# Performance work log

Hardware: AMD Instinct MI355X
Metric: run time of the kernel (lower is better)

The kernel has to match this reference:

```python
import jax, jax.numpy as jnp
import numpy as np

H, DK, DV, DEMB = 16, 64, 64, 1024
D_MODEL = H * DV


def setup_inputs() -> dict:
    key = jax.random.key(0)
    ks = jax.random.split(key, 9)
    scale = 0.02
    x = jax.random.normal(ks[0], (4, 2048, DEMB), dtype=jnp.float32)
    wq = jax.random.normal(ks[1], (DEMB, H * DK), dtype=jnp.float32) * scale
    bq = jnp.zeros((H * DK,), dtype=jnp.float32)
    wk = jax.random.normal(ks[2], (DEMB, H * DK), dtype=jnp.float32) * scale
    bk = jnp.zeros((H * DK,), dtype=jnp.float32)
    wv = jax.random.normal(ks[3], (DEMB, H * DV), dtype=jnp.float32) * scale
    bv = jnp.zeros((H * DV,), dtype=jnp.float32)
    wo = jax.random.normal(ks[4], (D_MODEL, D_MODEL), dtype=jnp.float32) * scale
    bo = jnp.zeros((D_MODEL,), dtype=jnp.float32)
    return {"x": x, "wq": wq, "bq": bq, "wk": wk, "bk": bk,
            "wv": wv, "bv": bv, "wo": wo, "bo": bo, "mask": 0}


def _split_heads(t, h):
    # (b, s, h*d) -> (b, h, s, d)
    b, s, _ = t.shape
    return t.reshape(b, s, h, -1).transpose(0, 2, 1, 3)


def reference(x, wq, bq, wk, bk, wv, bv, wo, bo, mask):
    b, s, _ = x.shape
    qs = _split_heads(x @ wq + bq, H)  # (b, h, s, dk)
    ks = _split_heads(x @ wk + bk, H)
    vs = _split_heads(x @ wv + bv, H)  # (b, h, s, dv)
    # FAITHFUL quirk: original scales by 1/sqrt(len(ks[0])) == 1/sqrt(n_heads),
    # not 1/sqrt(d_k).
    scores = jnp.einsum('bhqd,bhkd->bhqk', qs, ks) / jnp.sqrt(jnp.float32(H))
    # FAITHFUL quirk: masked_fill(mask == 0, ...) with scalar bool mask is a
    # no-op (True == 0 is False), so no masking is ever applied.
    attn = jax.nn.softmax(scores, axis=-1)
    out = jnp.einsum('bhqk,bhkd->bhqd', attn, vs)  # (b, h, s, dv)
    out = out.transpose(0, 2, 1, 3).reshape(b, s, D_MODEL)
    return out @ wo + bo
```

## Files before the change

kernel.cpp:

```cpp
#include <hip/hip_runtime.h>
#include <stdint.h>

typedef __attribute__((ext_vector_type(8))) short short8;
typedef __attribute__((ext_vector_type(4))) short short4v;
typedef __attribute__((ext_vector_type(4))) float floatx4;
typedef __attribute__((ext_vector_type(4))) _Float16 half4;
typedef __attribute__((ext_vector_type(2))) __fp16 pk2;

#define SEQ 2048
#define NTOK 8192
#define QSCALE 0.360673760222241f

#define MFMA16F16(a,b,c) __builtin_amdgcn_mfma_f32_16x16x16f16((a),(b),(c),0,0,0)

__device__ __forceinline__ float b2f(unsigned short u){
  union { unsigned int i; float f; } v; v.i = ((unsigned int)u) << 16; return v.f;
}
__device__ __forceinline__ unsigned short f2b(float f){
  union { float f; unsigned int i; } v; v.f = f;
  unsigned int r = v.i + 0x7fffu + ((v.i >> 16) & 1u);
  return (unsigned short)(r >> 16);
}
__device__ __forceinline__ void async16(const unsigned short* g, unsigned short* l){
  __builtin_amdgcn_global_load_lds(
      (const __attribute__((address_space(1))) unsigned int*)g,
      (__attribute__((address_space(3))) unsigned int*)l, 16, 0, 0);
}

__global__ __launch_bounds__(256) void convert_x_kernel(
    const float* __restrict__ src, unsigned short* __restrict__ dst)
{
  int i = (blockIdx.x*256 + threadIdx.x)*4;
  float4 v = *(const float4*)(src + i);
  short4v o;
  o[0] = (short)f2b(v.x); o[1] = (short)f2b(v.y);
  o[2] = (short)f2b(v.z); o[3] = (short)f2b(v.w);
  *(short4v*)(dst + i) = o;
}

__global__ __launch_bounds__(256) void transpose_w_kernel(
    const float* __restrict__ wq, const float* __restrict__ wk,
    const float* __restrict__ wv, const float* __restrict__ wo,
    unsigned short* __restrict__ wqkvT, unsigned short* __restrict__ woT)
{
  __shared__ unsigned short lT[64][72];
  const int sel = blockIdx.z;
  const float* src = (sel==0)?wq:(sel==1)?wk:(sel==2)?wv:wo;
  unsigned short* dst = (sel<3) ? (wqkvT + (size_t)sel*1024*1024) : woT;
  const int n0 = blockIdx.x * 64, k0 = blockIdx.y * 64;
  const int tid = threadIdx.x;
#pragma unroll
  for (int i=0;i<4;i++){
    int ch = tid + i*256;
    int r = ch>>4, c = (ch&15)*4;
    float4 v = *(const float4*)(src + (size_t)(k0+r)*1024 + n0 + c);
    lT[r][c+0] = f2b(v.x); lT[r][c+1] = f2b(v.y);
    lT[r][c+2] = f2b(v.z); lT[r][c+3] = f2b(v.w);
  }
  __syncthreads();
#pragma unroll
  for (int i=0;i<2;i++){
    int ch = tid + i*256;
    int rn = ch>>3, c = (ch&7)*8;
    short8 v;
#pragma unroll
    for (int j=0;j<8;j++) v[j] = (short)lT[c+j][rn];
    *(short8*)(dst + (size_t)(n0+rn)*1024 + k0 + c) = v;
  }
}

__global__ void bias_concat_kernel(const float* __restrict__ bq,
                                   const float* __restrict__ bk,
                                   const float* __restrict__ bv,
                                   float* __restrict__ bqkv){
  int i = blockIdx.x*256 + threadIdx.x;
  if (i < 3072){
    int sel = i >> 10, j = i & 1023;
    bqkv[i] = (sel==0)?bq[j]:(sel==1)?bk[j]:bv[j];
  }
}

template<int OUT_F32, int SCALE_Q>
__global__ __launch_bounds__(256) void gemm_bt_kernel(
    const unsigned short* __restrict__ A,
    const unsigned short* __restrict__ Bt,
    const float* __restrict__ bias,
    void* __restrict__ Cv,
    int M, int N, int K)
{
  __shared__ unsigned short lA[128*64];
  __shared__ unsigned short lB[128*64];
  const int tid  = threadIdx.x;
  const int lane = tid & 63;
  const int wave = tid >> 6;
  const int quad = lane >> 4;
  const int l15  = lane & 15;
  const int wR = (wave >> 1) * 64;
  const int wC = (wave & 1) * 64;
  const int rowB = blockIdx.y * 128;
  const int colB = blockIdx.x * 128;

  const int srow = wave*32 + (lane>>3);
  const int sc8  = (lane&7) ^ (lane>>3);
  const unsigned short* gA = A  + (size_t)(rowB + srow)*K + sc8*8;
  const unsigned short* gB = Bt + (size_t)(colB + srow)*K + sc8*8;
  unsigned short* lAw = lA + wave*32*64 + lane*8;
  unsigned short* lBw = lB + wave*32*64 + lane*8;

  floatx4 acc[4][4];
#pragma unroll
  for (int t=0;t<4;t++)
#pragma unroll
    for (int u=0;u<4;u++) acc[t][u] = (floatx4){0.f,0.f,0.f,0.f};

  for (int kt = 0; kt < K; kt += 64){
    __syncthreads();
#pragma unroll
    for (int i=0;i<4;i++){
      async16(gA + (size_t)i*8*K + kt, lAw + i*512);
      async16(gB + (size_t)i*8*K + kt, lBw + i*512);
    }
    __syncthreads();
#pragma unroll
    for (int ks=0; ks<2; ks++){
      const int cph = ((ks*4 + quad) ^ (l15 & 7)) * 8;
      short8 af[4], bf[4];
#pragma unroll
      for (int t=0;t<4;t++) af[t] = *(const short8*)&lA[(wR + t*16 + l15)*64 + cph];
#pragma unroll
      for (int u=0;u<4;u++) bf[u] = *(const short8*)&lB[(wC + u*16 + l15)*64 + cph];
#pragma unroll
      for (int t=0;t<4;t++)
#pragma unroll
        for (int u=0;u<4;u++)
          acc[t][u] = __builtin_amdgcn_mfma_f32_16x16x32_bf16(af[t], bf[u], acc[t][u], 0, 0, 0);
    }
  }
#pragma unroll
  for (int u=0;u<4;u++){
    int col = colB + wC + u*16 + l15;
    float bval = bias[col];
    float scale = (SCALE_Q && col < 1024) ? QSCALE : 1.0f;
#pragma unroll
    for (int t=0;t<4;t++){
      int row0 = rowB + wR + t*16 + quad*4;
#pragma unroll
      for (int r=0;r<4;r++){
        float val = (acc[t][u][r] + bval) * scale;
        if (OUT_F32) ((float*)Cv)[(size_t)(row0 + r)*N + col] = val;
        else ((unsigned short*)Cv)[(size_t)(row0 + r)*N + col] = f2b(val);
      }
    }
  }
}

__global__ __launch_bounds__(256) void transpose_v_kernel(
    const unsigned short* __restrict__ qkv,
    unsigned short* __restrict__ vt)
{
  __shared__ unsigned short lT[64][72];
  const int bh = blockIdx.x;
  const int b = bh >> 4, h = bh & 15;
  const int s0 = blockIdx.y * 64;
  const int tid = threadIdx.x;
#pragma unroll
  for (int i=0;i<2;i++){
    int ch = tid + i*256;
    int r = ch >> 3, c = (ch & 7)*8;
    short8 raw = *(const short8*)(qkv + (size_t)(b*SEQ + s0 + r)*3072 + 2048 + h*64 + c);
#pragma unroll
    for (int j=0;j<8;j++){
      union { _Float16 h; unsigned short u; } cv;
      cv.h = (_Float16)b2f((unsigned short)raw[j]);
      lT[r][c+j] = cv.u;
    }
  }
  __syncthreads();
#pragma unroll
  for (int i=0;i<2;i++){
    int ch = tid + i*256;
    int dv = ch >> 3, c = (ch & 7)*8;
    short8 v;
#pragma unroll
    for (int j=0;j<8;j++) v[j] = (short)lT[c+j][dv];
    *(short8*)(vt + (size_t)(bh*64 + dv)*2048 + s0 + c) = v;
  }
}

__global__ __launch_bounds__(256) void flash_attn_kernel(
    const unsigned short* __restrict__ qkv,
    const unsigned short* __restrict__ vt,
    unsigned short* __restrict__ attn_out)
{
  __shared__ unsigned short sK[64][72];
  __shared__ _Float16 sVt[64][72];
  const int bh = blockIdx.x;
  const int b = bh >> 4, h = bh & 15;
  const int qt = blockIdx.y;
  const int tid = threadIdx.x;
  const int wave = tid >> 6;
  const int lane = tid & 63;
  const int quad = lane >> 4, l15 = lane & 15;
  const int tok0 = b*SEQ + qt*128;

  short8 qf[2][2];
#pragma unroll
  for (int t=0;t<2;t++)
#pragma unroll
    for (int ks=0;ks<2;ks++)
      qf[t][ks] = *(const short8*)(qkv + (size_t)(tok0 + wave*32 + t*16 + l15)*3072
                                   + h*64 + ks*32 + quad*8);

  floatx4 oacc[2][4];
  float psum[2] = {0.f, 0.f};
#pragma unroll
  for (int t=0;t<2;t++)
#pragma unroll
    for (int v=0;v<4;v++) oacc[t][v] = (floatx4){0.f,0.f,0.f,0.f};

  const int ch0 = tid, ch1 = tid + 256;
  const int r0 = ch0 >> 3, c0 = (ch0 & 7)*8;
  const int r1 = ch1 >> 3, c1 = (ch1 & 7)*8;
  short8 rk[2], rv[2];
  rk[0] = *(const short8*)(qkv + (size_t)(b*SEQ + r0)*3072 + 1024 + h*64 + c0);
  rk[1] = *(const short8*)(qkv + (size_t)(b*SEQ + r1)*3072 + 1024 + h*64 + c1);
  rv[0] = *(const short8*)(vt  + (size_t)(bh*64 + r0)*2048 + c0);
  rv[1] = *(const short8*)(vt  + (size_t)(bh*64 + r1)*2048 + c1);

  for (int it = 0; it < SEQ/64; it++){
    __syncthreads();
    *(short8*)&sK[r0][c0]  = rk[0];
    *(short8*)&sK[r1][c1]  = rk[1];
    *(short8*)&sVt[r0][c0] = rv[0];
    *(short8*)&sVt[r1][c1] = rv[1];
    __syncthreads();
    if (it + 1 < SEQ/64){
      int itn = (it + 1) * 64;
      rk[0] = *(const short8*)(qkv + (size_t)(b*SEQ + itn + r0)*3072 + 1024 + h*64 + c0);
      rk[1] = *(const short8*)(qkv + (size_t)(b*SEQ + itn + r1)*3072 + 1024 + h*64 + c1);
      rv[0] = *(const short8*)(vt  + (size_t)(bh*64 + r0)*2048 + itn + c0);
      rv[1] = *(const short8*)(vt  + (size_t)(bh*64 + r1)*2048 + itn + c1);
    }

    floatx4 sacc[4][2];
#pragma unroll
    for (int u=0;u<4;u++)
#pragma unroll
      for (int t=0;t<2;t++) sacc[u][t] = (floatx4){0.f,0.f,0.f,0.f};
#pragma unroll
    for (int ks=0;ks<2;ks++){
      short8 kf[4];
#pragma unroll
      for (int u=0;u<4;u++) kf[u] = *(const short8*)&sK[u*16 + l15][ks*32 + quad*8];
#pragma unroll
      for (int u=0;u<4;u++)
#pragma unroll
        for (int t=0;t<2;t++)
          sacc[u][t] = __builtin_amdgcn_mfma_f32_16x16x32_bf16(kf[u], qf[t][ks], sacc[u][t], 0,0,0);
    }

    half4 pf[4][2];
#pragma unroll
    for (int t=0;t<2;t++){
#pragma unroll
      for (int u=0;u<4;u++){
        float p0 = __builtin_amdgcn_exp2f(sacc[u][t][0]);
        float p1 = __builtin_amdgcn_exp2f(sacc[u][t][1]);
        float p2 = __builtin_amdgcn_exp2f(sacc[u][t][2]);
        float p3 = __builtin_amdgcn_exp2f(sacc[u][t][3]);
        psum[t] += (p0+p1)+(p2+p3);
        union { pk2 p2v[2]; half4 h4; } cv;
        cv.p2v[0] = __builtin_amdgcn_cvt_pkrtz(p0,p1);
        cv.p2v[1] = __builtin_amdgcn_cvt_pkrtz(p2,p3);
        pf[u][t] = cv.h4;
      }
    }

#pragma unroll
    for (int v=0;v<4;v++){
      half4 vf[4];
#pragma unroll
      for (int u=0;u<4;u++) vf[u] = *(const half4*)&sVt[v*16 + l15][u*16 + quad*4];
#pragma unroll
      for (int t=0;t<2;t++)
#pragma unroll
        for (int u=0;u<4;u++)
          oacc[t][v] = MFMA16F16(pf[u][t], vf[u], oacc[t][v]);
    }
  }

#pragma unroll
  for (int t=0;t<2;t++){
    float s = psum[t];
    s += __shfl_xor(s, 16);
    s += __shfl_xor(s, 32);
    psum[t] = s;
  }
#pragma unroll
  for (int t=0;t<2;t++){
#pragma unroll
    for (int r=0;r<4;r++){
      float inv = 1.0f / __shfl(psum[t], quad*4 + r);
      int tok = tok0 + wave*32 + t*16 + quad*4 + r;
#pragma unroll
      for (int v=0;v<4;v++)
        attn_out[(size_t)tok*1024 + h*64 + v*16 + l15] = f2b(oacc[t][v][r] * inv);
    }
  }
}

extern "C" void kernel_launch(void* const* d_in, const int* in_sizes, int n_in,
                              void* d_out, int out_size, void* d_ws, size_t ws_size,
                              hipStream_t stream)
{
  const float* x  = (const float*)d_in[0];
  const float* wq = (const float*)d_in[1];
  const float* bq = (const float*)d_in[2];
  const float* wk = (const float*)d_in[3];
  const float* bk = (const float*)d_in[4];
  const float* wv = (const float*)d_in[5];
  const float* bv = (const float*)d_in[6];
  const float* wo = (const float*)d_in[7];
  const float* bo = (const float*)d_in[8];
  float* out = (float*)d_out;

  char* ws = (char*)d_ws;
  unsigned short* wqkvT  = (unsigned short*)(ws);
  unsigned short* woT    = (unsigned short*)(ws + 6291456);
  float*          bqkv   = (float*)(ws + 8388608);
  unsigned short* xb     = (unsigned short*)(ws + 8400896);
  unsigned short* qkvbuf = (unsigned short*)(ws + 25178112);
  unsigned short* vtbuf  = (unsigned short*)(ws + 75509760);
  unsigned short* aobuf  = (unsigned short*)(ws + 92286976);

  convert_x_kernel<<<dim3(8192), 256, 0, stream>>>(x, xb);
  transpose_w_kernel<<<dim3(16,16,4), 256, 0, stream>>>(wq, wk, wv, wo, wqkvT, woT);
  bias_concat_kernel<<<dim3(12), 256, 0, stream>>>(bq, bk, bv, bqkv);
  gemm_bt_kernel<0,1><<<dim3(24, 64), 256, 0, stream>>>(xb, wqkvT, bqkv, qkvbuf, 8192, 3072, 1024);
  transpose_v_kernel<<<dim3(64, 32), 256, 0, stream>>>(qkvbuf, vtbuf);
  flash_attn_kernel<<<dim3(64, 16), 256, 0, stream>>>(qkvbuf, vtbuf, aobuf);
  gemm_bt_kernel<1,0><<<dim3(8, 64), 256, 0, stream>>>(aobuf, woT, bo, out, 8192, 1024, 1024);
}
```

Before: 313.1 us.

## Double-buffer flash-attention K/V tiles via async LDS loads; merge prep kernels

The flash attention kernel now stages K and V^T tiles into two LDS buffers with direct global-to-LDS async loads, using an XOR-swizzled layout in place of padded rows. This cuts the register round trip and one of the two barriers per iteration, and lets the next tile's load overlap the current tile's MFMA work. Separately, the three prep kernels (x conversion, weight transpose, bias concat) are merged into one launch to save launch overhead. The changes double LDS use and depend on correct swizzle indexing and on the async loads being complete before the barrier.

```diff
diff --git a/kernel.cpp b/kernel.cpp
--- a/kernel.cpp
+++ b/kernel.cpp
@@ -27,56 +27,56 @@
       (__attribute__((address_space(3))) unsigned int*)l, 16, 0, 0);
 }
 
-__global__ __launch_bounds__(256) void convert_x_kernel(
-    const float* __restrict__ src, unsigned short* __restrict__ dst)
-{
-  int i = (blockIdx.x*256 + threadIdx.x)*4;
-  float4 v = *(const float4*)(src + i);
-  short4v o;
-  o[0] = (short)f2b(v.x); o[1] = (short)f2b(v.y);
-  o[2] = (short)f2b(v.z); o[3] = (short)f2b(v.w);
-  *(short4v*)(dst + i) = o;
-}
-
-__global__ __launch_bounds__(256) void transpose_w_kernel(
+__global__ __launch_bounds__(256) void prep_kernel(
+    const float* __restrict__ x,
     const float* __restrict__ wq, const float* __restrict__ wk,
     const float* __restrict__ wv, const float* __restrict__ wo,
-    unsigned short* __restrict__ wqkvT, unsigned short* __restrict__ woT)
+    const float* __restrict__ bq, const float* __restrict__ bk,
+    const float* __restrict__ bv,
+    unsigned short* __restrict__ xb,
+    unsigned short* __restrict__ wqkvT, unsigned short* __restrict__ woT,
+    float* __restrict__ bqkv)
 {
   __shared__ unsigned short lT[64][72];
-  const int sel = blockIdx.z;
-  const float* src = (sel==0)?wq:(sel==1)?wk:(sel==2)?wv:wo;
-  unsigned short* dst = (sel<3) ? (wqkvT + (size_t)sel*1024*1024) : woT;
-  const int n0 = blockIdx.x * 64, k0 = blockIdx.y * 64;
+  const int bid = blockIdx.x;
   const int tid = threadIdx.x;
-#pragma unroll
-  for (int i=0;i<4;i++){
-    int ch = tid + i*256;
-    int r = ch>>4, c = (ch&15)*4;
-    float4 v = *(const float4*)(src + (size_t)(k0+r)*1024 + n0 + c);
-    lT[r][c+0] = f2b(v.x); lT[r][c+1] = f2b(v.y);
-    lT[r][c+2] = f2b(v.z); lT[r][c+3] = f2b(v.w);
-  }
-  __syncthreads();
-#pragma unroll
-  for (int i=0;i<2;i++){
-    int ch = tid + i*256;
-    int rn = ch>>3, c = (ch&7)*8;
-    short8 v;
-#pragma unroll
-    for (int j=0;j<8;j++) v[j] = (short)lT[c+j][rn];
-    *(short8*)(dst + (size_t)(n0+rn)*1024 + k0 + c) = v;
-  }
-}
-
-__global__ void bias_concat_kernel(const float* __restrict__ bq,
-                                   const float* __restrict__ bk,
-                                   const float* __restrict__ bv,
-                                   float* __restrict__ bqkv){
-  int i = blockIdx.x*256 + threadIdx.x;
-  if (i < 3072){
-    int sel = i >> 10, j = i & 1023;
-    bqkv[i] = (sel==0)?bq[j]:(sel==1)?bk[j]:bv[j];
+  if (bid < 8192){
+    int i = (bid*256 + tid)*4;
+    float4 v = *(const float4*)(x + i);
+    short4v o;
+    o[0] = (short)f2b(v.x); o[1] = (short)f2b(v.y);
+    o[2] = (short)f2b(v.z); o[3] = (short)f2b(v.w);
+    *(short4v*)(xb + i) = o;
+  } else if (bid < 9216){
+    int idx = bid - 8192;
+    int sel = idx >> 8, rest = idx & 255;
+    const float* src = (sel==0)?wq:(sel==1)?wk:(sel==2)?wv:wo;
+    unsigned short* dst = (sel<3) ? (wqkvT + (size_t)sel*1024*1024) : woT;
+    int n0 = (rest & 15) * 64, k0 = (rest >> 4) * 64;
+#pragma unroll
+    for (int i=0;i<4;i++){
+      int ch = tid + i*256;
+      int r = ch>>4, c = (ch&15)*4;
+      float4 v = *(const float4*)(src + (size_t)(k0+r)*1024 + n0 + c);
+      lT[r][c+0] = f2b(v.x); lT[r][c+1] = f2b(v.y);
+      lT[r][c+2] = f2b(v.z); lT[r][c+3] = f2b(v.w);
+    }
+    __syncthreads();
+#pragma unroll
+    for (int i=0;i<2;i++){
+      int ch = tid + i*256;
+      int rn = ch>>3, c = (ch&7)*8;
+      short8 v;
+#pragma unroll
+      for (int j=0;j<8;j++) v[j] = (short)lT[c+j][rn];
+      *(short8*)(dst + (size_t)(n0+rn)*1024 + k0 + c) = v;
+    }
+  } else {
+    int i = (bid - 9216)*256 + tid;
+    if (i < 3072){
+      int sel = i >> 10, j = i & 1023;
+      bqkv[i] = (sel==0)?bq[j]:(sel==1)?bk[j]:bv[j];
+    }
   }
 }
 
@@ -192,8 +192,8 @@
     const unsigned short* __restrict__ vt,
     unsigned short* __restrict__ attn_out)
 {
-  __shared__ unsigned short sK[64][72];
-  __shared__ _Float16 sVt[64][72];
+  __shared__ unsigned short sK[2][64*64];
+  __shared__ _Float16 sV[2][64*64];
   const int bh = blockIdx.x;
   const int b = bh >> 4, h = bh & 15;
   const int qt = blockIdx.y;
@@ -203,6 +203,12 @@
   const int quad = lane >> 4, l15 = lane & 15;
   const int tok0 = b*SEQ + qt*128;
 
+  const int srow = lane >> 3;
+  const int sc8  = (lane & 7) ^ srow;
+  const unsigned short* gK = qkv + (size_t)(b*SEQ + wave*16 + srow)*3072 + 1024 + h*64 + sc8*8;
+  const unsigned short* gV = vt  + (size_t)(bh*64 + wave*16 + srow)*2048 + sc8*8;
+  const int ldso = (wave*16)*64 + lane*8;
+
   short8 qf[2][2];
 #pragma unroll
   for (int t=0;t<2;t++)
@@ -218,28 +224,22 @@
 #pragma unroll
     for (int v=0;v<4;v++) oacc[t][v] = (floatx4){0.f,0.f,0.f,0.f};
 
-  const int ch0 = tid, ch1 = tid + 256;
-  const int r0 = ch0 >> 3, c0 = (ch0 & 7)*8;
-  const int r1 = ch1 >> 3, c1 = (ch1 & 7)*8;
-  short8 rk[2], rv[2];
-  rk[0] = *(const short8*)(qkv + (size_t)(b*SEQ + r0)*3072 + 1024 + h*64 + c0);
-  rk[1] = *(const short8*)(qkv + (size_t)(b*SEQ + r1)*3072 + 1024 + h*64 + c1);
-  rv[0] = *(const short8*)(vt  + (size_t)(bh*64 + r0)*2048 + c0);
-  rv[1] = *(const short8*)(vt  + (size_t)(bh*64 + r1)*2048 + c1);
+#pragma unroll
+  for (int i=0;i<2;i++){
+    async16(gK + (size_t)i*8*3072, &sK[0][ldso + i*512]);
+    async16(gV + (size_t)i*8*2048, (unsigned short*)&sV[0][ldso + i*512]);
+  }
+  __syncthreads();
 
   for (int it = 0; it < SEQ/64; it++){
-    __syncthreads();
-    *(short8*)&sK[r0][c0]  = rk[0];
-    *(short8*)&sK[r1][c1]  = rk[1];
-    *(short8*)&sVt[r0][c0] = rv[0];
-    *(short8*)&sVt[r1][c1] = rv[1];
-    __syncthreads();
+    const int bi = it & 1;
     if (it + 1 < SEQ/64){
-      int itn = (it + 1) * 64;
-      rk[0] = *(const short8*)(qkv + (size_t)(b*SEQ + itn + r0)*3072 + 1024 + h*64 + c0);
-      rk[1] = *(const short8*)(qkv + (size_t)(b*SEQ + itn + r1)*3072 + 1024 + h*64 + c1);
-      rv[0] = *(const short8*)(vt  + (size_t)(bh*64 + r0)*2048 + itn + c0);
-      rv[1] = *(const short8*)(vt  + (size_t)(bh*64 + r1)*2048 + itn + c1);
+      const int nx = (it + 1) * 64;
+#pragma unroll
+      for (int i=0;i<2;i++){
+        async16(gK + (size_t)(i*8 + (size_t)nx)*3072, &sK[bi^1][ldso + i*512]);
+        async16(gV + (size_t)i*8*2048 + nx, (unsigned short*)&sV[bi^1][ldso + i*512]);
+      }
     }
 
     floatx4 sacc[4][2];
@@ -249,9 +249,10 @@
       for (int t=0;t<2;t++) sacc[u][t] = (floatx4){0.f,0.f,0.f,0.f};
 #pragma unroll
     for (int ks=0;ks<2;ks++){
+      const int cph = ((ks*4 + quad) ^ (l15 & 7)) * 8;
       short8 kf[4];
 #pragma unroll
-      for (int u=0;u<4;u++) kf[u] = *(const short8*)&sK[u*16 + l15][ks*32 + quad*8];
+      for (int u=0;u<4;u++) kf[u] = *(const short8*)&sK[bi][(u*16 + l15)*64 + cph];
 #pragma unroll
       for (int u=0;u<4;u++)
 #pragma unroll
@@ -280,13 +281,17 @@
     for (int v=0;v<4;v++){
       half4 vf[4];
 #pragma unroll
-      for (int u=0;u<4;u++) vf[u] = *(const half4*)&sVt[v*16 + l15][u*16 + quad*4];
+      for (int u=0;u<4;u++){
+        const int cph = ((2*u + (quad>>1)) ^ (l15 & 7)) * 8 + (quad&1)*4;
+        vf[u] = *(const half4*)&sV[bi][(v*16 + l15)*64 + cph];
+      }
 #pragma unroll
       for (int t=0;t<2;t++)
 #pragma unroll
         for (int u=0;u<4;u++)
           oacc[t][v] = MFMA16F16(pf[u][t], vf[u], oacc[t][v]);
     }
+    __syncthreads();
   }
 
 #pragma unroll
@@ -333,9 +338,8 @@
   unsigned short* vtbuf  = (unsigned short*)(ws + 75509760);
   unsigned short* aobuf  = (unsigned short*)(ws + 92286976);
 
-  convert_x_kernel<<<dim3(8192), 256, 0, stream>>>(x, xb);
-  transpose_w_kernel<<<dim3(16,16,4), 256, 0, stream>>>(wq, wk, wv, wo, wqkvT, woT);
-  bias_concat_kernel<<<dim3(12), 256, 0, stream>>>(bq, bk, bv, bqkv);
+  prep_kernel<<<dim3(9228), 256, 0, stream>>>(x, wq, wk, wv, wo, bq, bk, bv,
+                                              xb, wqkvT, woT, bqkv);
   gemm_bt_kernel<0,1><<<dim3(24, 64), 256, 0, stream>>>(xb, wqkvT, bqkv, qkvbuf, 8192, 3072, 1024);
   transpose_v_kernel<<<dim3(64, 32), 256, 0, stream>>>(qkvbuf, vtbuf);
   flash_attn_kernel<<<dim3(64, 16), 256, 0, stream>>>(qkvbuf, vtbuf, aobuf);
```

After: 314.9 us. No clear change (+0.6%).
